# Optimization experiments

Measured on AMD Instinct MI355X. Metric: run time of the kernel, lower is better.

## Reference

```python
import jax, jax.numpy as jnp
import numpy as np

B, T, D, H, L = 64, 512, 1024, 1024, 4


def setup_inputs() -> dict:
    key = jax.random.key(0)
    ks = jax.random.split(key, 5)
    scale = 1.0 / np.sqrt(H)
    return {
        "x": jax.random.normal(ks[0], (B, T, D), dtype=jnp.float32),
        "Wih": jax.random.normal(ks[1], (L, 4 * H, D), dtype=jnp.float32) * scale,
        "Whh": jax.random.normal(ks[2], (L, 4 * H, H), dtype=jnp.float32) * scale,
        "bih": jax.random.normal(ks[3], (L, 4 * H), dtype=jnp.float32) * scale,
        "bhh": jax.random.normal(ks[4], (L, 4 * H), dtype=jnp.float32) * scale,
    }


def _lstm_layer(x_tbd, Wih, Whh, b):
    # x_tbd: [T, B, in]; Wih: [4H, in]; Whh: [4H, H]; b: [4H]
    Bsz = x_tbd.shape[1]
    Hsz = Whh.shape[1]
    # precompute the input-side GEMM for the whole sequence in one shot
    xg = jnp.einsum('tbd,gd->tbg', x_tbd, Wih) + b  # [T, B, 4H]

    def step(carry, xg_t):
        h, c = carry
        z = xg_t + h @ Whh.T  # [B, 4H]
        i, f, g, o = jnp.split(z, 4, axis=-1)  # torch LSTMCell gate order
        c = jax.nn.sigmoid(f) * c + jax.nn.sigmoid(i) * jnp.tanh(g)
        h = jax.nn.sigmoid(o) * jnp.tanh(c)
        return (h, c), h

    init = (jnp.zeros((Bsz, Hsz), x_tbd.dtype), jnp.zeros((Bsz, Hsz), x_tbd.dtype))
    (h_last, _), hs = jax.lax.scan(step, init, xg)
    return hs, h_last  # hs: [T, B, H]


def reference(x, Wih, Whh, bih, bhh):
    # layer-by-layer over the stack (fixed small L); each layer scans over time
    seq = jnp.transpose(x, (1, 0, 2))  # [T, B, D]
    h_last = None
    for l in range(L):
        seq, h_last = _lstm_layer(seq, Wih[l], Whh[l], bih[l] + bhh[l])
    return h_last  # [B, output_size], hidden of last layer at final timestep
```

## Files before the change

kernel.cpp:

```cpp
#include <hip/hip_runtime.h>
#include <math.h>


#define BSZ 64
#define TSZ 512
#define DSZ 1024
#define HSZ 1024
#define LSZ 4
#define NBLK 256
#define NTHR 512
#define NSTEP (TSZ + LSZ - 1)
#define BUFB 32768

typedef _Float16 half8  __attribute__((ext_vector_type(8)));
typedef _Float16 half4  __attribute__((ext_vector_type(4)));
typedef _Float16 half2v __attribute__((ext_vector_type(2)));
typedef float    f32x4  __attribute__((ext_vector_type(4)));
typedef float    f32x8  __attribute__((ext_vector_type(8)));

constexpr size_t N_X  = (size_t)BSZ * TSZ * DSZ;
constexpr size_t N_H  = (size_t)2 * LSZ * BSZ * HSZ;
constexpr size_t OFF_X     = 0;
constexpr size_t OFF_H     = OFF_X + N_X * 2;
constexpr size_t OFF_FLAGS = OFF_H + N_H * 2;
constexpr size_t OFF_GEN   = OFF_FLAGS + (size_t)NBLK * 64;
constexpr size_t BAR_BYTES = (size_t)NBLK * 64 + 64;

__device__ inline float fsig(float x) {
  return __builtin_amdgcn_rcpf(1.0f + __expf(-x));
}
__device__ inline float ftanh(float x) {
  float e = __expf(fminf(2.0f * x, 80.0f));
  return 1.0f - 2.0f * __builtin_amdgcn_rcpf(e + 1.0f);
}

__device__ inline void gload16(const void* g, void* l) {
  __builtin_amdgcn_global_load_lds(
      (const __attribute__((address_space(1))) void*)g,
      (__attribute__((address_space(3))) void*)l, 16, 0, 0);
}

__device__ inline void gbar(unsigned* flags, unsigned* gen, unsigned tgt) {
  __syncthreads();
  if (blockIdx.x == 0) {
    const int t = threadIdx.x;
    if (t >= 1 && t < NBLK) {
      while (__hip_atomic_load(&flags[t * 16], __ATOMIC_RELAXED,
                               __HIP_MEMORY_SCOPE_AGENT) < tgt)
        __builtin_amdgcn_s_sleep(2);
    }
    __syncthreads();
    if (t == 0) {
      __hip_atomic_store(gen, tgt, __ATOMIC_RELAXED, __HIP_MEMORY_SCOPE_AGENT);
      __builtin_amdgcn_fence(__ATOMIC_ACQUIRE, "agent");
    }
  } else {
    if (threadIdx.x == 0) {
      __hip_atomic_store(&flags[(size_t)blockIdx.x * 16], tgt, __ATOMIC_RELAXED,
                         __HIP_MEMORY_SCOPE_AGENT);
      while (__hip_atomic_load(gen, __ATOMIC_RELAXED,
                               __HIP_MEMORY_SCOPE_AGENT) < tgt)
        __builtin_amdgcn_s_sleep(2);
      __builtin_amdgcn_fence(__ATOMIC_ACQUIRE, "agent");
    }
  }
  __syncthreads();
}

__global__ __launch_bounds__(NTHR, 1) void lstm_persistent(
    const float* __restrict__ xin, const float* __restrict__ Wih,
    const float* __restrict__ Whh, const float* __restrict__ bih,
    const float* __restrict__ bhh, float* __restrict__ out,
    char* __restrict__ ws)
{
  _Float16* x16   = (_Float16*)(ws + OFF_X);
  _Float16* h16   = (_Float16*)(ws + OFF_H);
  unsigned* flags = (unsigned*)(ws + OFF_FLAGS);
  unsigned* gen   = (unsigned*)(ws + OFF_GEN);

  const int tid  = threadIdx.x;
  const int gtid = blockIdx.x * NTHR + tid;
  const int lane = tid & 63;
  const int w    = tid >> 6;
  const int mat  = w >> 2;
  const int rp   = (w >> 1) & 1;
  const int kh   = w & 1;
  const int ln15 = lane & 15;
  const int lq   = lane >> 4;

  const int l  = blockIdx.x >> 6;
  const int cc = blockIdx.x & 63;
  const int c0 = cc * 16;

  const float* Wsel = mat ? Whh : Wih;
  half8 bw[2][16];
#pragma unroll
  for (int gl = 0; gl < 2; ++gl) {
    const float* wrow =
        Wsel + (size_t)(l * 4096 + (rp * 2 + gl) * 1024 + c0 + ln15) * 1024 +
        kh * 512;
#pragma unroll
    for (int ks = 0; ks < 16; ++ks) {
      f32x8 f = *(const f32x8*)(wrow + ks * 32 + lq * 8);
      bw[gl][ks] = __builtin_convertvector(f, half8);
    }
  }

  const int gb = tid >> 3;
  const int gc = (tid & 7) * 2;
  float bsg[4][2];
#pragma unroll
  for (int g = 0; g < 4; ++g) {
    const int bb = l * 4096 + g * 1024 + c0 + gc;
    bsg[g][0] = bih[bb] + bhh[bb];
    bsg[g][1] = bih[bb + 1] + bhh[bb + 1];
  }
  float cr0 = 0.f, cr1 = 0.f;

  const int sb   = tid >> 3;
  const int pswl = ((tid & 7) ^ (sb & 7)) << 4;
  const int dstb = (tid >> 6) << 10;

  {
    const f32x4* s4 = (const f32x4*)xin;
    unsigned long long* xu = (unsigned long long*)x16;
    const int dq = DSZ / 4;
    for (int i = gtid; i < (int)(N_X / 4); i += NBLK * NTHR) {
      const int d4  = i & (dq - 1);
      const int rem = i >> 8;
      const int tt  = rem & (TSZ - 1);
      const int bb  = rem >> 9;
      half4 v = __builtin_convertvector(s4[i], half4);
      const size_t o = ((size_t)tt * BSZ + bb) * dq + d4;
      __hip_atomic_store(&xu[o], __builtin_bit_cast(unsigned long long, v),
                         __ATOMIC_RELAXED, __HIP_MEMORY_SCOPE_AGENT);
    }
    unsigned long long* hz = (unsigned long long*)h16;
    for (int i = gtid; i < (int)(N_H / 4); i += NBLK * NTHR)
      __hip_atomic_store(&hz[i], 0ull, __ATOMIC_RELAXED,
                         __HIP_MEMORY_SCOPE_AGENT);
  }
  unsigned btgt = 1;
  gbar(flags, gen, btgt++);

  __shared__ __align__(16) char smem[2 * BUFB];
  float* pl = (float*)smem;

  const int lm1 = (l > 0) ? (l - 1) : 0;

  for (int s = 0; s < NSTEP; ++s) {
    const int t = s - l;
    if (t >= 0 && t < TSZ) {
      const int prevslot = (s + 1) & 1;
      const _Float16* hin  = h16 + (size_t)prevslot * (LSZ * BSZ * HSZ) +
                             (size_t)lm1 * (BSZ * HSZ);
      const _Float16* hown = h16 + (size_t)prevslot * (LSZ * BSZ * HSZ) +
                             (size_t)l * (BSZ * HSZ);
      const _Float16* base0 = (l == 0) ? x16 + (size_t)t * (BSZ * DSZ) : hin;

      const char* p0 = (const char*)(base0 + (size_t)sb * 1024) + pswl;
      const char* p1 = (const char*)(hown + (size_t)sb * HSZ) + pswl;

      auto stage = [&](int kc, int bsel) {
        const char* r0 = p0 + kc * 128;
        const char* r1 = p1 + kc * 128;
        char* d = smem + bsel * BUFB + dstb;
        gload16(r0,        d);
        gload16(r0 + 1024, d + 8192);
        gload16(r1,        d + 16384);
        gload16(r1 + 1024, d + 24576);
      };

      f32x4 acc[4][2] = {};

      stage(0, 0);
      __syncthreads();

      const int rdoff = mat * 16384 + kh * 8192;
#pragma unroll
      for (int kc = 0; kc < 8; ++kc) {
        if (kc < 7) stage(kc + 1, (kc + 1) & 1);
        const char* rdb = smem + (kc & 1) * BUFB + rdoff;
#pragma unroll
        for (int ksl = 0; ksl < 2; ++ksl) {
#pragma unroll
          for (int mt = 0; mt < 4; ++mt) {
            const int row = mt * 16 + ln15;
            const half8 a = *(const half8*)(rdb + row * 128 +
                                            ((ksl * 64 + lq * 16) ^
                                             ((row & 7) << 4)));
            acc[mt][0] = __builtin_amdgcn_mfma_f32_16x16x32_f16(
                a, bw[0][kc * 2 + ksl], acc[mt][0], 0, 0, 0);
            acc[mt][1] = __builtin_amdgcn_mfma_f32_16x16x32_f16(
                a, bw[1][kc * 2 + ksl], acc[mt][1], 0, 0, 0);
          }
        }
        __syncthreads();
      }

      if (l == 0 && t + 1 < TSZ) {
        const char* xnext =
            (const char*)(x16 + (size_t)(t + 1) * (BSZ * DSZ)) +
            ((cc >> 3) & 7) * 16384;
        char* trash = smem + BUFB + dstb;
        gload16(xnext + tid * 16, trash);
        gload16(xnext + 8192 + tid * 16, trash);
      }

      if (mat == 0) {
#pragma unroll
        for (int mt = 0; mt < 4; ++mt)
#pragma unroll
          for (int gl = 0; gl < 2; ++gl) {
            const int v  = (rp * 2 + gl) * 16 + ln15;
            const int bp = (mt * 16 + lq * 4) ^ ((ln15 & 7) << 2);
            *(f32x4*)&pl[kh * 4096 + v * 64 + bp] = acc[mt][gl];
          }
      }
      __syncthreads();
      if (mat == 1) {
#pragma unroll
        for (int mt = 0; mt < 4; ++mt)
#pragma unroll
          for (int gl = 0; gl < 2; ++gl) {
            const int v  = (rp * 2 + gl) * 16 + ln15;
            const int bp = (mt * 16 + lq * 4) ^ ((ln15 & 7) << 2);
            f32x4* p = (f32x4*)&pl[kh * 4096 + v * 64 + bp];
            *p = *p + acc[mt][gl];
          }
      }
      __syncthreads();

      {
        float z[4][2];
#pragma unroll
        for (int g = 0; g < 4; ++g)
#pragma unroll
          for (int j = 0; j < 2; ++j) {
            const int v  = g * 16 + gc + j;
            const int bp = gb ^ ((v & 7) << 2);
            z[g][j] = pl[0 * 4096 + v * 64 + bp] +
                      pl[1 * 4096 + v * 64 + bp] + bsg[g][j];
          }
        float cn0 = fsig(z[1][0]) * cr0 + fsig(z[0][0]) * ftanh(z[2][0]);
        float cn1 = fsig(z[1][1]) * cr1 + fsig(z[0][1]) * ftanh(z[2][1]);
        float hn0 = fsig(z[3][0]) * ftanh(cn0);
        float hn1 = fsig(z[3][1]) * ftanh(cn1);
        cr0 = cn0; cr1 = cn1;
        half2v hv; hv[0] = (_Float16)hn0; hv[1] = (_Float16)hn1;
        const size_t ho = (size_t)(s & 1) * (LSZ * BSZ * HSZ) +
                          (size_t)l * (BSZ * HSZ) + (size_t)gb * HSZ + c0 + gc;
        __hip_atomic_store((unsigned*)(h16 + ho),
                           __builtin_bit_cast(unsigned, hv),
                           __ATOMIC_RELAXED, __HIP_MEMORY_SCOPE_AGENT);
        if (l == LSZ - 1 && t == TSZ - 1) {
          out[(size_t)gb * HSZ + c0 + gc]     = hn0;
          out[(size_t)gb * HSZ + c0 + gc + 1] = hn1;
        }
      }
    }
    gbar(flags, gen, btgt++);
  }
}

extern "C" void kernel_launch(void* const* d_in, const int* in_sizes, int n_in,
                              void* d_out, int out_size, void* d_ws, size_t ws_size,
                              hipStream_t stream) {
  const float* x   = (const float*)d_in[0];
  const float* Wih = (const float*)d_in[1];
  const float* Whh = (const float*)d_in[2];
  const float* bih = (const float*)d_in[3];
  const float* bhh = (const float*)d_in[4];
  float* out = (float*)d_out;
  char*  ws  = (char*)d_ws;

  hipMemsetAsync(ws + OFF_FLAGS, 0, BAR_BYTES, stream);

  void* args[] = {(void*)&x, (void*)&Wih, (void*)&Whh, (void*)&bih,
                  (void*)&bhh, (void*)&out, (void*)&ws};
  hipLaunchCooperativeKernel((const void*)lstm_persistent, dim3(NBLK), dim3(NTHR),
                             args, 0, stream);
}
```

Measured before the change: 4.778 ms.

## Triple-buffer K-chunk staging with counted waits and single-pass partial reduction

Switches the LDS staging of input and hidden tiles from double to triple buffering with a prefetch distance of two. Plain __syncthreads are replaced by explicit vmcnt waits plus s_barrier, so up to one chunk of global loads stays in flight across each barrier. Each mat/kh wave group now writes its partials to its own LDS slice, and the gate step sums four slices, removing a store/barrier/add round. LDS use grows to 96KB per block, which may limit occupancy, and the hand-written waitcnt values must match the load count exactly.

Measured after the change: 4.563 ms. 4.5% less time.

```diff
diff --git a/kernel.cpp b/kernel.cpp
--- a/kernel.cpp
+++ b/kernel.cpp
@@ -143,7 +143,7 @@
   unsigned btgt = 1;
   gbar(flags, gen, btgt++);
 
-  __shared__ __align__(16) char smem[2 * BUFB];
+  __shared__ __align__(16) char smem[3 * BUFB];
   float* pl = (float*)smem;
 
   const int lm1 = (l > 0) ? (l - 1) : 0;
@@ -174,13 +174,17 @@
       f32x4 acc[4][2] = {};
 
       stage(0, 0);
-      __syncthreads();
+      stage(1, 1);
+      __builtin_amdgcn_sched_barrier(0);
+      asm volatile("s_waitcnt vmcnt(4)" ::: "memory");
+      __builtin_amdgcn_s_barrier();
+      __builtin_amdgcn_sched_barrier(0);
 
       const int rdoff = mat * 16384 + kh * 8192;
 #pragma unroll
       for (int kc = 0; kc < 8; ++kc) {
-        if (kc < 7) stage(kc + 1, (kc + 1) & 1);
-        const char* rdb = smem + (kc & 1) * BUFB + rdoff;
+        if (kc + 2 < 8) stage(kc + 2, (kc + 2) % 3);
+        const char* rdb = smem + (kc % 3) * BUFB + rdoff;
 #pragma unroll
         for (int ksl = 0; ksl < 2; ++ksl) {
 #pragma unroll
@@ -195,41 +199,37 @@
                 a, bw[1][kc * 2 + ksl], acc[mt][1], 0, 0, 0);
           }
         }
-        __syncthreads();
+        __builtin_amdgcn_sched_barrier(0);
+        if (kc <= 5)      asm volatile("s_waitcnt vmcnt(4)" ::: "memory");
+        else if (kc == 6) asm volatile("s_waitcnt vmcnt(0)" ::: "memory");
+        __builtin_amdgcn_s_barrier();
+        __builtin_amdgcn_sched_barrier(0);
       }
 
       if (l == 0 && t + 1 < TSZ) {
         const char* xnext =
             (const char*)(x16 + (size_t)(t + 1) * (BSZ * DSZ)) +
             ((cc >> 3) & 7) * 16384;
-        char* trash = smem + BUFB + dstb;
+        char* trash = smem + 2 * BUFB + dstb;
         gload16(xnext + tid * 16, trash);
         gload16(xnext + 8192 + tid * 16, trash);
       }
 
-      if (mat == 0) {
+      {
+        const int pbase = (mat * 2 + kh) * 4096;
 #pragma unroll
         for (int mt = 0; mt < 4; ++mt)
 #pragma unroll
           for (int gl = 0; gl < 2; ++gl) {
             const int v  = (rp * 2 + gl) * 16 + ln15;
             const int bp = (mt * 16 + lq * 4) ^ ((ln15 & 7) << 2);
-            *(f32x4*)&pl[kh * 4096 + v * 64 + bp] = acc[mt][gl];
+            *(f32x4*)&pl[pbase + v * 64 + bp] = acc[mt][gl];
           }
       }
-      __syncthreads();
-      if (mat == 1) {
-#pragma unroll
-        for (int mt = 0; mt < 4; ++mt)
-#pragma unroll
-          for (int gl = 0; gl < 2; ++gl) {
-            const int v  = (rp * 2 + gl) * 16 + ln15;
-            const int bp = (mt * 16 + lq * 4) ^ ((ln15 & 7) << 2);
-            f32x4* p = (f32x4*)&pl[kh * 4096 + v * 64 + bp];
-            *p = *p + acc[mt][gl];
-          }
-      }
-      __syncthreads();
+      __builtin_amdgcn_sched_barrier(0);
+      asm volatile("s_waitcnt lgkmcnt(0)" ::: "memory");
+      __builtin_amdgcn_s_barrier();
+      __builtin_amdgcn_sched_barrier(0);
 
       {
         float z[4][2];
@@ -240,7 +240,9 @@
             const int v  = g * 16 + gc + j;
             const int bp = gb ^ ((v & 7) << 2);
             z[g][j] = pl[0 * 4096 + v * 64 + bp] +
-                      pl[1 * 4096 + v * 64 + bp] + bsg[g][j];
+                      pl[1 * 4096 + v * 64 + bp] +
+                      pl[2 * 4096 + v * 64 + bp] +
+                      pl[3 * 4096 + v * 64 + bp] + bsg[g][j];
           }
         float cn0 = fsig(z[1][0]) * cr0 + fsig(z[0][0]) * ftanh(z[2][0]);
         float cn1 = fsig(z[1][1]) * cr1 + fsig(z[0][1]) * ftanh(z[2][1]);
```
